# Kernel tuning notes

Hardware: AMD Instinct MI355X
Metric: run time of the kernel (lower is better)

The kernel has to match this reference:

```python
import jax, jax.numpy as jnp
import numpy as np

H = 16   # num_heads
G = 4    # groups (code structurally requires 4)
DIM = 1024
HD = DIM // H // G  # 16


def setup_inputs() -> dict:
    key = jax.random.key(0)
    k1, k2, k3 = jax.random.split(key, 3)
    x = jax.random.normal(k1, (8, 4096, DIM), dtype=jnp.float32)
    w_qkvw = jax.random.normal(k2, (DIM, 4 * DIM), dtype=jnp.float32) * 0.02
    w_out = jax.random.normal(k3, (DIM, DIM), dtype=jnp.float32) * 0.02
    return {"x": x, "w_qkvw": w_qkvw, "w_out": w_out}


def reference(x, w_qkvw, w_out):
    B, S, dim = x.shape
    qkvw = x @ w_qkvw  # [B, S, 4*dim]
    # chunk into G groups along last dim -> G tensors of [B, S, dim] (G==4)
    chunks = jnp.split(qkvw, G, axis=-1)
    # each chunk split again into G sub-chunks of [B, S, dim/G]
    subs = [jnp.split(t, G, axis=-1) for t in chunks]
    # torch: q,k,v,w = [cat([qi,ki,vi,wi], dim=0) for qi,ki,vi,wi in zip(*subs)]
    q = jnp.concatenate([subs[i][0] for i in range(4)], axis=0)  # [4B, S, dim/G]
    k = jnp.concatenate([subs[i][1] for i in range(4)], axis=0)
    v = jnp.concatenate([subs[i][2] for i in range(4)], axis=0)
    w = jnp.concatenate([subs[i][3] for i in range(4)], axis=0)
    # faithful row-major reshape: [4B, S, dim/G] -> [4B, H, S, hd] -> transpose(1,2)
    def shp(t):
        return t.reshape(B * G, H, -1, HD).swapaxes(1, 2)  # [4B, S, H, hd]
    q, k, v = shp(q), shp(k), shp(v)
    w = w.reshape(B * G, H, -1, HD)  # [4B, H, S, hd]
    scale = HD ** -0.5
    scores = (q @ k.swapaxes(-2, -1)) * scale          # [4B, S, H, H]
    attn = jax.nn.softmax(scores, axis=-1)
    o = (attn @ v).swapaxes(1, 2).reshape(B, S, dim)   # [B, S, dim]
    return (o * w.reshape(B, S, dim)) @ w_out
```

## Files before the change

kernel.cpp:

```cpp
#include <hip/hip_runtime.h>
#include <hip/hip_bf16.h>
#include <stdint.h>


typedef __bf16 bf16;
typedef __bf16 bf16x8 __attribute__((ext_vector_type(8)));
typedef float f32x4 __attribute__((ext_vector_type(4)));

__device__ __forceinline__ void gload16(const bf16* g, bf16* l) {
  __builtin_amdgcn_global_load_lds(
      (const __attribute__((address_space(1))) void*)g,
      (__attribute__((address_space(3))) void*)l, 16, 0, 0);
}

#define BAR() __builtin_amdgcn_s_barrier()
#define SB() __builtin_amdgcn_sched_barrier(0)
#define LGKM8 asm volatile("s_waitcnt lgkmcnt(8)" ::: "memory")
#define LGKM4 asm volatile("s_waitcnt lgkmcnt(4)" ::: "memory")
#define LGKM0 asm volatile("s_waitcnt lgkmcnt(0)" ::: "memory")
#define VM4 asm volatile("s_waitcnt vmcnt(4)" ::: "memory")
#define VM0 asm volatile("s_waitcnt vmcnt(0)" ::: "memory")
#define PRIO1 __builtin_amdgcn_s_setprio(1)
#define PRIO0 __builtin_amdgcn_s_setprio(0)

#define READ_A8(dst, base, mq)                                                \
  {                                                                           \
    _Pragma("unroll") for (int i = 0; i < 4; ++i)                             \
        _Pragma("unroll") for (int kk = 0; kk < 2; ++kk)                      \
            dst[i][kk] = *(const bf16x8*)(lds + (base) + ahalf +              \
                                          ((mq)*64 + i * 16 + fr) * 128 +     \
                                          ((kk * 64 + fkb) ^ xo));            \
  }
#define READ_B4(dst, base, nh)                                                \
  {                                                                           \
    _Pragma("unroll") for (int j2 = 0; j2 < 2; ++j2)                          \
        _Pragma("unroll") for (int kk = 0; kk < 2; ++kk)                      \
            dst[j2][kk] = *(const bf16x8*)(lds + (base) + bhalf +             \
                                           (bro + (nh)*32 + j2 * 16 + fr) * 128 + \
                                           ((kk * 64 + fkb) ^ xo));           \
  }
#define MFMA_Q(arr, bv, mq, nh)                                               \
  {                                                                           \
    _Pragma("unroll") for (int i = 0; i < 4; ++i)                             \
        _Pragma("unroll") for (int j2 = 0; j2 < 2; ++j2) {                    \
      acc[(mq)*4 + i][(nh)*2 + j2] = __builtin_amdgcn_mfma_f32_16x16x32_bf16( \
          arr[i][0], bv[j2][0], acc[(mq)*4 + i][(nh)*2 + j2], 0, 0, 0);       \
      acc[(mq)*4 + i][(nh)*2 + j2] = __builtin_amdgcn_mfma_f32_16x16x32_bf16( \
          arr[i][1], bv[j2][1], acc[(mq)*4 + i][(nh)*2 + j2], 0, 0, 0);       \
    }                                                                         \
  }
#define STAGE(gsrc, lbase)                                                    \
  {                                                                           \
    gload16((gsrc), (bf16*)(lds + (lbase) + wv * 1024));                      \
    gload16((gsrc) + 64 * 1024, (bf16*)(lds + (lbase) + 8192 + wv * 1024));   \
  }

template <typename OutT>
__global__ __launch_bounds__(512, 2)
void gemm256(const bf16* __restrict__ A, const bf16* __restrict__ BT,
             OutT* __restrict__ C, int N, int super) {
  constexpr int K = 1024;
  __shared__ __align__(16) char smem[131072];
  char* lds = smem;

  const int tid = threadIdx.x;
  const int lane = tid & 63;
  const int wv = tid >> 6;
  const int wr = wv >> 2;
  const int wc = wv & 3;

  const int gx = gridDim.x;
  const int nwg = gx * gridDim.y;
  const int bid = blockIdx.y * gx + blockIdx.x;
  const int xcd = bid & 7;
  const int l = bid >> 3;
  long trow, tcol;
  if (super) {
    const int s = l >> 5, i = l & 31;
    const int colS = gx >> 2;
    trow = xcd * 16 + (s / colS) * 8 + (i >> 2);
    tcol = (s % colS) * 4 + (i & 3);
  } else {
    const int swz = xcd * (nwg >> 3) + l;
    trow = swz / gx;
    tcol = swz % gx;
  }
  const long row0 = trow * 256;
  const long col0 = tcol * 256;

  const int srow = tid >> 3;
  const int scol = (((tid & 7) * 16) ^ ((srow & 7) << 4)) >> 1;
  const bf16* gA = A + (row0 + srow) * K + scol;
  const bf16* gB = BT + (col0 + srow) * K + scol;

  const int fr = lane & 15;
  const int fkb = (lane >> 4) * 16;
  const int xo = (fr & 7) << 4;
  const int bro = (wc & 1) * 64;
  const int ahalf = wr * 16384;
  const int bhalf = (wc >> 1) * 16384;

  bf16x8 a0[4][2], a1[4][2], bn0[2][2], bn1[2][2];
  f32x4 acc[8][4] = {};

  STAGE(gA, 0); STAGE(gA + 131072, 16384);
  STAGE(gB, 65536); STAGE(gB + 131072, 81920);
  STAGE(gA + 64, 32768); STAGE(gA + 131072 + 64, 49152);
  VM4;

  const bf16* gAm = gA;
  const bf16* gBm = gB;
  for (int j = 0; j < 8; ++j) {
    const bool nl = (j < 7);
    BAR();
    READ_B4(bn0, 65536, 0);
    READ_A8(a0, 0, 0);
    READ_A8(a1, 0, 1);
    STAGE(gBm + 64, 98304);
    LGKM8; SB();
    PRIO1; MFMA_Q(a0, bn0, 0, 0); PRIO0;
    BAR();
    READ_B4(bn1, 65536, 1);
    STAGE(gBm + 131072 + 64, 114688);
    LGKM4; SB();
    PRIO1; MFMA_Q(a1, bn0, 1, 0); PRIO0;
    BAR();
    if (nl) STAGE(gAm + 128, 0);
    LGKM0; SB();
    PRIO1; MFMA_Q(a1, bn1, 1, 1); PRIO0;
    BAR();
    if (nl) {
      STAGE(gAm + 131072 + 128, 16384);
      VM4;
    } else {
      VM0;
    }
    SB();
    PRIO1; MFMA_Q(a0, bn1, 0, 1); PRIO0;
    BAR();
    READ_B4(bn0, 98304, 0);
    READ_A8(a0, 32768, 0);
    READ_A8(a1, 32768, 1);
    if (nl) STAGE(gBm + 128, 65536);
    LGKM8; SB();
    PRIO1; MFMA_Q(a0, bn0, 0, 0); PRIO0;
    BAR();
    READ_B4(bn1, 98304, 1);
    if (nl) STAGE(gBm + 131072 + 128, 81920);
    LGKM4; SB();
    PRIO1; MFMA_Q(a1, bn0, 1, 0); PRIO0;
    BAR();
    if (nl) STAGE(gAm + 192, 32768);
    LGKM0; SB();
    PRIO1; MFMA_Q(a1, bn1, 1, 1); PRIO0;
    BAR();
    if (nl) {
      STAGE(gAm + 131072 + 192, 49152);
      VM4;
    }
    SB();
    PRIO1; MFMA_Q(a0, bn1, 0, 1); PRIO0;
    gAm += 128;
    gBm += 128;
  }

  const int crow = (lane >> 4) * 4;
  const int ccol = lane & 15;
  const long rb = row0 + wr * 128;
  const long cb = col0 + wc * 64;
#pragma unroll
  for (int m = 0; m < 8; ++m)
#pragma unroll
    for (int n = 0; n < 4; ++n)
#pragma unroll
      for (int i = 0; i < 4; ++i)
        C[(rb + m * 16 + crow + i) * (long)N + cb + n * 16 + ccol] =
            (OutT)acc[m][n][i];
}

__device__ __forceinline__ void load16f(const bf16* p, float* f) {
  const uint4* u = (const uint4*)p;
  uint4 a = u[0], b = u[1];
  uint32_t w[8] = {a.x, a.y, a.z, a.w, b.x, b.y, b.z, b.w};
#pragma unroll
  for (int j = 0; j < 8; ++j) {
    f[2 * j] = __uint_as_float(w[j] << 16);
    f[2 * j + 1] = __uint_as_float(w[j] & 0xffff0000u);
  }
}

__global__ __launch_bounds__(256)
void attn_fuse(const bf16* __restrict__ qkvw, bf16* __restrict__ ow,
               int b0, long bstride) {
  __shared__ bf16 data[16 * 1024];
  const int s_hi = blockIdx.x;
  const int g = blockIdx.y;
  const int bz = blockIdx.z;
  const int b = b0 + bz;
  const bf16* base = qkvw + (long)bz * bstride;
  const int tid = threadIdx.x;

#pragma unroll
  for (int i = 0; i < 8; ++i) {
    int c = tid + i * 256;
    int h = c >> 7;
    int col = (c & 127) * 8;
    *(uint4*)&data[h * 1024 + col] =
        *(const uint4*)(base + (long)(h * 256 + s_hi) * 4096 + g * 1024 + col);
  }
  __syncthreads();

  const int s_lo = tid >> 4;
  const int h1 = tid & 15;
  const int off = s_lo * 16;

  float q[16], p[16], o[16];
  load16f(&data[h1 * 1024 + off], q);

  float mx = -1e30f;
#pragma unroll
  for (int h2 = 0; h2 < 16; ++h2) {
    float kf[16];
    load16f(&data[h2 * 1024 + 256 + off], kf);
    float s = 0.f;
#pragma unroll
    for (int d = 0; d < 16; ++d) s += q[d] * kf[d];
    s *= 0.25f;
    p[h2] = s;
    mx = fmaxf(mx, s);
  }
  float sum = 0.f;
#pragma unroll
  for (int h2 = 0; h2 < 16; ++h2) {
    float e = __expf(p[h2] - mx);
    p[h2] = e;
    sum += e;
  }
  const float inv = 1.f / sum;
#pragma unroll
  for (int d = 0; d < 16; ++d) o[d] = 0.f;
#pragma unroll
  for (int h2 = 0; h2 < 16; ++h2) {
    float vf[16];
    load16f(&data[h2 * 1024 + 512 + off], vf);
    const float av = p[h2] * inv;
#pragma unroll
    for (int d = 0; d < 16; ++d) o[d] += av * vf[d];
  }
  float wf[16];
  load16f(&data[h1 * 1024 + 768 + off], wf);

  const int bp = g * 8 + b;
  const long R = (long)(bp >> 2) * 4096 + (bp & 3) * 1024 + h1 * 64 + (s_hi >> 2);
  const int cbo = (s_hi & 3) * 256 + off;
  union { uint4 u[2]; bf16 hh[16]; } st;
#pragma unroll
  for (int d = 0; d < 16; ++d) st.hh[d] = (bf16)(o[d] * wf[d]);
  uint4* dst = (uint4*)&ow[R * 1024 + cbo];
  dst[0] = st.u[0];
  dst[1] = st.u[1];
}

__global__ __launch_bounds__(256)
void cast_x_kernel(const float* __restrict__ in, bf16* __restrict__ out, long n4) {
  long i = (long)blockIdx.x * 256 + threadIdx.x;
  if (i >= n4) return;
  float4 v = ((const float4*)in)[i];
  union { uint2 d; bf16 h[4]; } r;
  r.h[0] = (bf16)v.x; r.h[1] = (bf16)v.y; r.h[2] = (bf16)v.z; r.h[3] = (bf16)v.w;
  ((uint2*)out)[i] = r.d;
}

__global__ __launch_bounds__(256)
void tcast_kernel(const float* __restrict__ in, bf16* __restrict__ out, int R, int C) {
  __shared__ float t[64][65];
  const int c0 = blockIdx.x * 64, r0 = blockIdx.y * 64;
  const int lr = threadIdx.x >> 6;
  const int lc = threadIdx.x & 63;
#pragma unroll
  for (int i = 0; i < 16; ++i)
    t[lr + i * 4][lc] = in[(long)(r0 + lr + i * 4) * C + c0 + lc];
  __syncthreads();
#pragma unroll
  for (int i = 0; i < 16; ++i) {
    int oc = lr + i * 4;
    out[(long)(c0 + oc) * R + r0 + lc] = (bf16)t[lc][oc];
  }
}

extern "C" void kernel_launch(void* const* d_in, const int* in_sizes, int n_in,
                              void* d_out, int out_size, void* d_ws, size_t ws_size,
                              hipStream_t stream) {
  const float* x = (const float*)d_in[0];
  const float* w_qkvw = (const float*)d_in[1];
  const float* w_out = (const float*)d_in[2];
  float* out = (float*)d_out;

  char* ws = (char*)d_ws;
  size_t off = 0;
  bf16* x_bf = (bf16*)(ws + off); off += (size_t)32768 * 1024 * 2;
  bf16* bt1  = (bf16*)(ws + off); off += (size_t)4096 * 1024 * 2;
  bf16* bt2  = (bf16*)(ws + off); off += (size_t)1024 * 1024 * 2;
  bf16* owb  = (bf16*)(ws + off); off += (size_t)32768 * 1024 * 2;
  bf16* qk   = (bf16*)(ws + off);
  const size_t rem = ws_size > off ? ws_size - off : 0;
  const size_t full_need = (size_t)32768 * 4096 * 2;

  cast_x_kernel<<<32768, 256, 0, stream>>>(x, x_bf, (long)8388608);
  tcast_kernel<<<dim3(64, 16), 256, 0, stream>>>(w_qkvw, bt1, 1024, 4096);
  tcast_kernel<<<dim3(16, 16), 256, 0, stream>>>(w_out, bt2, 1024, 1024);

  if (rem >= full_need) {
    gemm256<bf16><<<dim3(16, 128), 512, 0, stream>>>(x_bf, bt1, qk, 4096, 1);
    attn_fuse<<<dim3(256, 4, 8), 256, 0, stream>>>(qk, owb, 0, (long)4096 * 4096);
  } else {
    for (int b = 0; b < 8; ++b) {
      gemm256<bf16><<<dim3(16, 16), 512, 0, stream>>>(
          x_bf + (size_t)b * 4096 * 1024, bt1, qk, 4096, 0);
      attn_fuse<<<dim3(256, 4, 1), 256, 0, stream>>>(qk, owb, b, 0);
    }
  }
  gemm256<float><<<dim3(4, 128), 512, 0, stream>>>(owb, bt2, out, 1024, 1);
}
```

Baseline: 452.9 us.

## Replace fine-grained interleaved GEMM pipeline with simpler two-stage double buffer

Restructures the GEMM main loop from an 8-phase schedule, in which global-to-LDS stages are interleaved between MFMA quarters with barriers and partial vmcnt waits, into a two-stage ping-pong. Each half-iteration issues all loads for the other buffer, reads all fragments with staged lgkmcnt waits, and runs the four MFMA quarters. This cuts the number of barriers per iteration. The cost is full vmcnt(0) waits, which may expose global load latency that the old schedule hid behind compute.

```diff
diff --git a/kernel.cpp b/kernel.cpp
--- a/kernel.cpp
+++ b/kernel.cpp
@@ -15,10 +15,9 @@
 
 #define BAR() __builtin_amdgcn_s_barrier()
 #define SB() __builtin_amdgcn_sched_barrier(0)
+#define LGKM12 asm volatile("s_waitcnt lgkmcnt(12)" ::: "memory")
 #define LGKM8 asm volatile("s_waitcnt lgkmcnt(8)" ::: "memory")
-#define LGKM4 asm volatile("s_waitcnt lgkmcnt(4)" ::: "memory")
 #define LGKM0 asm volatile("s_waitcnt lgkmcnt(0)" ::: "memory")
-#define VM4 asm volatile("s_waitcnt vmcnt(4)" ::: "memory")
 #define VM0 asm volatile("s_waitcnt vmcnt(0)" ::: "memory")
 #define PRIO1 __builtin_amdgcn_s_setprio(1)
 #define PRIO0 __builtin_amdgcn_s_setprio(0)
@@ -53,6 +52,22 @@
   {                                                                           \
     gload16((gsrc), (bf16*)(lds + (lbase) + wv * 1024));                      \
     gload16((gsrc) + 64 * 1024, (bf16*)(lds + (lbase) + 8192 + wv * 1024));   \
+  }
+
+#define TILE_BODY(AB, BB)                                                     \
+  {                                                                           \
+    READ_B4(bn0, BB, 0);                                                      \
+    READ_A8(a0, AB, 0);                                                       \
+    SB();                                                                     \
+    READ_B4(bn1, BB, 1);                                                      \
+    SB();                                                                     \
+    READ_A8(a1, AB, 1);                                                       \
+    LGKM12; SB();                                                             \
+    PRIO1; MFMA_Q(a0, bn0, 0, 0); PRIO0;                                      \
+    LGKM8; SB();                                                              \
+    PRIO1; MFMA_Q(a0, bn1, 0, 1); PRIO0;                                      \
+    LGKM0; SB();                                                              \
+    PRIO1; MFMA_Q(a1, bn0, 1, 0); MFMA_Q(a1, bn1, 1, 1); PRIO0;               \
   }
 
 template <typename OutT>
@@ -105,61 +120,24 @@
 
   STAGE(gA, 0); STAGE(gA + 131072, 16384);
   STAGE(gB, 65536); STAGE(gB + 131072, 81920);
-  STAGE(gA + 64, 32768); STAGE(gA + 131072 + 64, 49152);
-  VM4;
+  VM0;
 
   const bf16* gAm = gA;
   const bf16* gBm = gB;
   for (int j = 0; j < 8; ++j) {
     const bool nl = (j < 7);
     BAR();
-    READ_B4(bn0, 65536, 0);
-    READ_A8(a0, 0, 0);
-    READ_A8(a1, 0, 1);
-    STAGE(gBm + 64, 98304);
-    LGKM8; SB();
-    PRIO1; MFMA_Q(a0, bn0, 0, 0); PRIO0;
-    BAR();
-    READ_B4(bn1, 65536, 1);
-    STAGE(gBm + 131072 + 64, 114688);
-    LGKM4; SB();
-    PRIO1; MFMA_Q(a1, bn0, 1, 0); PRIO0;
-    BAR();
-    if (nl) STAGE(gAm + 128, 0);
-    LGKM0; SB();
-    PRIO1; MFMA_Q(a1, bn1, 1, 1); PRIO0;
+    STAGE(gAm + 64, 32768); STAGE(gAm + 131072 + 64, 49152);
+    STAGE(gBm + 64, 98304); STAGE(gBm + 131072 + 64, 114688);
+    TILE_BODY(0, 65536);
+    VM0;
     BAR();
     if (nl) {
-      STAGE(gAm + 131072 + 128, 16384);
-      VM4;
-    } else {
-      VM0;
+      STAGE(gAm + 128, 0); STAGE(gAm + 131072 + 128, 16384);
+      STAGE(gBm + 128, 65536); STAGE(gBm + 131072 + 128, 81920);
     }
-    SB();
-    PRIO1; MFMA_Q(a0, bn1, 0, 1); PRIO0;
-    BAR();
-    READ_B4(bn0, 98304, 0);
-    READ_A8(a0, 32768, 0);
-    READ_A8(a1, 32768, 1);
-    if (nl) STAGE(gBm + 128, 65536);
-    LGKM8; SB();
-    PRIO1; MFMA_Q(a0, bn0, 0, 0); PRIO0;
-    BAR();
-    READ_B4(bn1, 98304, 1);
-    if (nl) STAGE(gBm + 131072 + 128, 81920);
-    LGKM4; SB();
-    PRIO1; MFMA_Q(a1, bn0, 1, 0); PRIO0;
-    BAR();
-    if (nl) STAGE(gAm + 192, 32768);
-    LGKM0; SB();
-    PRIO1; MFMA_Q(a1, bn1, 1, 1); PRIO0;
-    BAR();
-    if (nl) {
-      STAGE(gAm + 131072 + 192, 49152);
-      VM4;
-    }
-    SB();
-    PRIO1; MFMA_Q(a0, bn1, 0, 1); PRIO0;
+    TILE_BODY(32768, 98304);
+    if (nl) VM0;
     gAm += 128;
     gBm += 128;
   }
```

New measurement: 465.3 us. 2.8% more time.
